# Performance work log

Measured on AMD Instinct MI355X. Metric: run time of the kernel, lower is better.

## Reference

```python
import jax, jax.numpy as jnp
import numpy as np

DIM, HEADS, K = 128, 4, 7
HD = DIM // HEADS


def _nbr_idx(n, k):
    # NATTEN boundary-clamped neighborhood (dilation=1): window start clamped to [0, n-k]
    i = np.arange(n)
    start = np.clip(i - k // 2, 0, n - k)
    idx = start[:, None] + np.arange(k)[None, :]          # (n, k) absolute neighbor index
    rel = idx - i[:, None] + (k - 1)                      # (n, k) index into 2k-1 rpb axis
    return jnp.asarray(idx), jnp.asarray(rel)


def _ln(x, w, b, eps=1e-5):
    mu = jnp.mean(x, -1, keepdims=True)
    var = jnp.var(x, -1, keepdims=True)
    return (x - mu) * jax.lax.rsqrt(var + eps) * w + b


def setup_inputs() -> dict:
    key = jax.random.key(0)
    ks = jax.random.split(key, 16)
    B, H, W, C = 1, 128, 128, DIM
    f = jax.random.normal
    inp = {
        'x': f(ks[0], (B, H, W, C), jnp.float32),
        'y': f(ks[1], (B, H, W, C), jnp.float32),
        'qv_w': f(ks[2], (2 * C, C), jnp.float32) * 0.02,
        'qv_b': jnp.zeros((2 * C,), jnp.float32),
        'k_w': f(ks[3], (C, C), jnp.float32) * 0.02,
        'k_b': jnp.zeros((C,), jnp.float32),
        'rpb': f(ks[4], (HEADS, 2 * K - 1, 2 * K - 1), jnp.float32) * 0.02,
        'proj_w': f(ks[5], (C, C), jnp.float32) * 0.02,
        'proj_b': jnp.zeros((C,), jnp.float32),
        'n1_w': jnp.ones((C,), jnp.float32),
        'n1_b': jnp.zeros((C,), jnp.float32),
        'n2_w': jnp.ones((C,), jnp.float32),
        'n2_b': jnp.zeros((C,), jnp.float32),
        'fc1_w': f(ks[6], (4 * C, C), jnp.float32) * 0.02,
        'fc1_b': jnp.zeros((4 * C,), jnp.float32),
        'fc2_w': f(ks[7], (C, 4 * C), jnp.float32) * 0.02,
        'fc2_b': jnp.zeros((C,), jnp.float32),
    }
    return inp


def _block(x, y, qv_w, qv_b, k_w, k_b, rpb, proj_w, proj_b,
           n1_w, n1_b, n2_w, n2_b, fc1_w, fc1_b, fc2_w, fc2_b):
    B, H, W, C = x.shape
    scale = HD ** -0.5
    # ---- CrossNat2D attention on norm1(x) vs y ----
    xn = _ln(x, n1_w, n1_b)
    qv = xn @ qv_w.T + qv_b                               # (B,H,W,2C)
    q = qv[..., :C].reshape(B, H, W, HEADS, HD) * scale
    v = qv[..., C:].reshape(B, H, W, HEADS, HD)
    k = (y @ k_w.T + k_b).reshape(B, H, W, HEADS, HD)

    idx_h, rel_h = _nbr_idx(H, K)
    idx_w, rel_w = _nbr_idx(W, K)
    # gather neighborhoods: (B, H, K, W, K, HEADS, HD)
    k_nbr = k[:, idx_h][:, :, :, idx_w]
    v_nbr = v[:, idx_h][:, :, :, idx_w]

    # attention logits over KxK neighborhood
    attn = jnp.einsum('bijhd,biajchd->bijhac', q, k_nbr)  # (B,H,W,heads,K,K)
    bias = rpb[:, rel_h][..., rel_w]                      # (heads,H,K,W,K)
    attn = attn + jnp.transpose(bias, (1, 3, 0, 2, 4))    # broadcast over B
    attn = jax.nn.softmax(attn.reshape(B, H, W, HEADS, K * K), axis=-1)
    attn = attn.reshape(B, H, W, HEADS, K, K)

    out = jnp.einsum('bijhac,biajchd->bijhd', attn, v_nbr).reshape(B, H, W, C)
    out = out @ proj_w.T + proj_b

    x = x + out
    # ---- MLP ----
    h = _ln(x, n2_w, n2_b) @ fc1_w.T + fc1_b
    h = jax.nn.gelu(h, approximate=False) @ fc2_w.T + fc2_b
    return x + h


def reference(x, y, qv_w, qv_b, k_w, k_b, rpb, proj_w, proj_b,
              n1_w, n1_b, n2_w, n2_b, fc1_w, fc1_b, fc2_w, fc2_b):
    return _block(x, y, qv_w, qv_b, k_w, k_b, rpb, proj_w, proj_b,
                  n1_w, n1_b, n2_w, n2_b, fc1_w, fc1_b, fc2_w, fc2_b)
```

## Files before the change

kernel.cpp:

```cpp
#include <hip/hip_runtime.h>
#include <hip/hip_bf16.h>


#define N_PIX 16384
#define C 128
#define HEADS 4
#define HD 32
#define HW 128

typedef __hip_bfloat16 bf16;
typedef __attribute__((ext_vector_type(8))) short bf16x8;
typedef __attribute__((ext_vector_type(4))) float f32x4;

__device__ __forceinline__ short f2bs(float f) {
    bf16 h = __float2bfloat16(f);
    return (short)__bfloat16_as_ushort(h);
}
__device__ __forceinline__ float bs2f(short s) {
    __hip_bfloat16_raw r; r.x = (unsigned short)s;
    return __bfloat162float(__hip_bfloat16(r));
}
__device__ __forceinline__ float gelu_f(float v) {
    const float z = 1.5957691216f * (v + 0.044715f * v * v * v);
    return v / (1.f + __expf(-z));
}
__device__ __forceinline__ unsigned int pack2(float a, float b) {
    return (unsigned int)(unsigned short)f2bs(a) |
           ((unsigned int)(unsigned short)f2bs(b) << 16);
}

__global__ __launch_bounds__(256) void k_wconv(
    const float* __restrict__ qv_w, const float* __restrict__ k_w,
    const float* __restrict__ proj_w, const float* __restrict__ fc1_w,
    const float* __restrict__ fc2_w,
    short* __restrict__ wqv, short* __restrict__ wk, short* __restrict__ wproj,
    short* __restrict__ wfc1, short* __restrict__ wfc2) {
    const int i = blockIdx.x * 256 + threadIdx.x;
    if (i < 32768) wqv[i] = f2bs(qv_w[i]);
    if (i < 16384) { wk[i] = f2bs(k_w[i]); wproj[i] = f2bs(proj_w[i]); }
    if (i < 65536) { wfc1[i] = f2bs(fc1_w[i]); wfc2[i] = f2bs(fc2_w[i]); }
}

__global__ __launch_bounds__(256, 4) void k_qkv(
    const float* __restrict__ x, const float* __restrict__ y,
    const short* __restrict__ wqv, const float* __restrict__ qv_b,
    const short* __restrict__ wk, const float* __restrict__ k_b,
    const float* __restrict__ n1_w, const float* __restrict__ n1_b,
    bf16* __restrict__ qb, bf16* __restrict__ vb, bf16* __restrict__ kb) {
    __shared__ float xr[16][132];
    __shared__ short xn[16][136];
    __shared__ short yl[16][136];
    __shared__ float muA[16], riA[16];
    const int t = threadIdx.x;
    const int pix0 = (blockIdx.x & 7) * 2048 + (blockIdx.x >> 3) * 16;
    for (int e = t; e < 512; e += 256) {
        const int r = e >> 5, c4 = (e & 31) * 4;
        const float4 xv = *(const float4*)(x + (size_t)(pix0 + r) * C + c4);
        *(float4*)&xr[r][c4] = xv;
        const float4 yv = *(const float4*)(y + (size_t)(pix0 + r) * C + c4);
        uint2 yp; yp.x = pack2(yv.x, yv.y); yp.y = pack2(yv.z, yv.w);
        *(uint2*)&yl[r][c4] = yp;
    }
    __syncthreads();
    if (t < 128) {
        const int r = t >> 3, s = t & 7;
        float sm = 0.f, sq = 0.f;
        for (int i = 0; i < 16; i++) { float v = xr[r][s * 16 + i]; sm += v; sq += v * v; }
        for (int m = 1; m < 8; m <<= 1) { sm += __shfl_xor(sm, m, 64); sq += __shfl_xor(sq, m, 64); }
        if (s == 0) {
            const float mu = sm * (1.f / 128.f);
            const float var = sq * (1.f / 128.f) - mu * mu;
            muA[r] = mu; riA[r] = rsqrtf(var + 1e-5f);
        }
    }
    __syncthreads();
    for (int e = t; e < 2048; e += 256) {
        const int r = e >> 7, c = e & 127;
        xn[r][c] = f2bs((xr[r][c] - muA[r]) * riA[r] * n1_w[c] + n1_b[c]);
    }
    __syncthreads();
    const int wave = t >> 6, lane = t & 63, quad = lane >> 4, l15 = lane & 15;
    const float scale = 0.1767766952966369f;
    {
        bf16x8 aA[4];
#pragma unroll
        for (int kt = 0; kt < 4; kt++)
            aA[kt] = *(const bf16x8*)&xn[l15][kt * 32 + quad * 8];
#pragma unroll
        for (int s = 0; s < 4; s++) {
            const int n = (wave * 4 + s) * 16 + l15;
            f32x4 acc = {0.f, 0.f, 0.f, 0.f};
#pragma unroll
            for (int kt = 0; kt < 4; kt++) {
                bf16x8 b = *(const bf16x8*)&wqv[n * C + kt * 32 + quad * 8];
                acc = __builtin_amdgcn_mfma_f32_16x16x32_bf16(aA[kt], b, acc, 0, 0, 0);
            }
            const float bias = qv_b[n];
#pragma unroll
            for (int r = 0; r < 4; r++) {
                const int m = quad * 4 + r;
                const float v = acc[r] + bias;
                if (n < C) qb[(size_t)(pix0 + m) * C + n] = __float2bfloat16(v * scale);
                else       vb[(size_t)(pix0 + m) * C + (n - C)] = __float2bfloat16(v);
            }
        }
    }
    {
        bf16x8 aY[4];
#pragma unroll
        for (int kt = 0; kt < 4; kt++)
            aY[kt] = *(const bf16x8*)&yl[l15][kt * 32 + quad * 8];
        const int n0 = (wave * 2) * 16 + l15, n1 = (wave * 2 + 1) * 16 + l15;
        f32x4 a0 = {0.f, 0.f, 0.f, 0.f}, a1 = {0.f, 0.f, 0.f, 0.f};
#pragma unroll
        for (int kt = 0; kt < 4; kt++) {
            bf16x8 b0 = *(const bf16x8*)&wk[n0 * C + kt * 32 + quad * 8];
            bf16x8 b1 = *(const bf16x8*)&wk[n1 * C + kt * 32 + quad * 8];
            a0 = __builtin_amdgcn_mfma_f32_16x16x32_bf16(aY[kt], b0, a0, 0, 0, 0);
            a1 = __builtin_amdgcn_mfma_f32_16x16x32_bf16(aY[kt], b1, a1, 0, 0, 0);
        }
        const float b0s = k_b[n0], b1s = k_b[n1];
#pragma unroll
        for (int r = 0; r < 4; r++) {
            const int m = quad * 4 + r;
            kb[(size_t)(pix0 + m) * C + n0] = __float2bfloat16(a0[r] + b0s);
            kb[(size_t)(pix0 + m) * C + n1] = __float2bfloat16(a1[r] + b1s);
        }
    }
}

__global__ __launch_bounds__(512, 2) void k_fam(
    const bf16* __restrict__ qb, const bf16* __restrict__ kb,
    const bf16* __restrict__ vb, const float* __restrict__ rpb,
    const float* __restrict__ x,
    const short* __restrict__ wproj, const float* __restrict__ proj_b,
    const float* __restrict__ n2_w, const float* __restrict__ n2_b,
    const short* __restrict__ wfc1, const float* __restrict__ fc1_b,
    const short* __restrict__ wfc2, const float* __restrict__ fc2_b,
    float* __restrict__ out) {
    __shared__ short KP[19008];
    __shared__ short Vl[19008];
    __shared__ float muA[32], riA[32];
    short* const Pm  = KP;
    short* const aoL = KP;
    short* const x1b = KP + 4352;
    short* const xnb = KP + 8704;
    short* const hb  = Vl;
    const int t = threadIdx.x;
    const int wave = t >> 6, lane = t & 63, quad = lane >> 4, l15 = lane & 15;
    const int h = wave & 3, mt = wave >> 2;
    const int s_ = blockIdx.x >> 3;
    const int i0 = ((blockIdx.x & 7) * 2 + (s_ >> 5)) * 8;
    const int j0 = (s_ & 31) * 4;
    const int rs = min(max(i0 - 3, 0), 114);
    const int cs = min(max(j0 - 3, 0), 118);
    const int mA = mt * 16 + l15;
    const int pA = (i0 + (mA >> 2)) * HW + j0 + (mA & 3);
    const bf16x8 aQ = *(const bf16x8*)(qb + (size_t)pA * C + h * HD + quad * 8);
    const int nR0 = h * 16 + l15, nR1 = (h + 4) * 16 + l15;
    float xres0[4], xres1[4];
#pragma unroll
    for (int r = 0; r < 4; r++) {
        const int m = mt * 16 + quad * 4 + r;
        const int p = (i0 + (m >> 2)) * HW + j0 + (m & 3);
        xres0[r] = x[(size_t)p * C + nR0];
        xres1[r] = x[(size_t)p * C + nR1];
    }
    for (int u = t; u < 140 * 16 * 2; u += 512) {
        const int tv = (u >= 2240) ? 1 : 0;
        const int uu = tv ? u - 2240 : u;
        const int r = uu >> 4, seg = uu & 15;
        const size_t g = (size_t)((rs + r / 10) * HW + cs + r % 10) * C + seg * 8;
        const uint4 d = *(const uint4*)((tv ? vb : kb) + g);
        *(uint4*)&(tv ? Vl : KP)[r * 132 + seg * 8] = d;
    }
    __syncthreads();
    f32x4 S[9];
#pragma unroll
    for (int nt = 0; nt < 9; nt++) {
        const bf16x8 bK = *(const bf16x8*)&KP[(nt * 16 + l15) * 132 + h * HD + quad * 8];
        f32x4 z = {0.f, 0.f, 0.f, 0.f};
        S[nt] = __builtin_amdgcn_mfma_f32_16x16x32_bf16(aQ, bK, z, 0, 0, 0);
    }
    const float* rpbh = rpb + h * 169;
    float smx[4];
#pragma unroll
    for (int r = 0; r < 4; r++) {
        const int m = mt * 16 + quad * 4 + r;
        const int i = i0 + (m >> 2), j = j0 + (m & 3);
        const int shi = min(max(i - 3, 0), 121);
        const int swj = min(max(j - 3, 0), 121);
        float best = -1e30f;
#pragma unroll
        for (int nt = 0; nt < 9; nt++) {
            const int nb = nt * 16 + l15;
            const int ai = rs + nb / 10, aj = cs + nb % 10;
            const bool valid = (nb < 140) & (ai >= shi) & (ai <= shi + 6) & (aj >= swj) & (aj <= swj + 6);
            const int ri = min(max(ai - i + 6, 0), 12);
            const int rj = min(max(aj - j + 6, 0), 12);
            const float v = valid ? (S[nt][r] + rpbh[ri * 13 + rj]) : -1e30f;
            S[nt][r] = v;
            best = fmaxf(best, v);
        }
        for (int msk = 1; msk < 16; msk <<= 1) best = fmaxf(best, __shfl_xor(best, msk, 64));
        float s = 0.f;
#pragma unroll
        for (int nt = 0; nt < 9; nt++) {
            const float e = __expf(S[nt][r] - best);
            S[nt][r] = e;
            s += e;
        }
        for (int msk = 1; msk < 16; msk <<= 1) s += __shfl_xor(s, msk, 64);
        smx[r] = 1.f / s;
    }
    __syncthreads();
#pragma unroll
    for (int r = 0; r < 4; r++) {
        short* prow = &Pm[(wave * 16 + quad * 4 + r) * 144];
#pragma unroll
        for (int nt = 0; nt < 9; nt++)
            prow[nt * 16 + l15] = f2bs(S[nt][r] * smx[r]);
    }
    f32x4 O0 = {0.f, 0.f, 0.f, 0.f}, O1 = {0.f, 0.f, 0.f, 0.f};
#pragma unroll
    for (int kt = 0; kt < 4; kt++) {
        const bf16x8 aP = *(const bf16x8*)&Pm[(wave * 16 + l15) * 144 + kt * 32 + quad * 8];
#pragma unroll
        for (int nt2 = 0; nt2 < 2; nt2++) {
            const int ch = h * HD + nt2 * 16 + l15;
            const int base = (kt * 32 + quad * 8) * 132 + ch;
            bf16x8 bV;
#pragma unroll
            for (int jj = 0; jj < 8; jj++) bV[jj] = Vl[base + jj * 132];
            if (nt2 == 0) O0 = __builtin_amdgcn_mfma_f32_16x16x32_bf16(aP, bV, O0, 0, 0, 0);
            else          O1 = __builtin_amdgcn_mfma_f32_16x16x32_bf16(aP, bV, O1, 0, 0, 0);
        }
    }
    {
        const bf16x8 aP = *(const bf16x8*)&Pm[(wave * 16 + l15) * 144 + 128 + quad * 8];
#pragma unroll
        for (int nt2 = 0; nt2 < 2; nt2++) {
            const int ch = h * HD + nt2 * 16 + l15;
            bf16x8 bV = {0, 0, 0, 0, 0, 0, 0, 0};
            if (quad == 0) {
                const int base = 128 * 132 + ch;
#pragma unroll
                for (int jj = 0; jj < 8; jj++) bV[jj] = Vl[base + jj * 132];
            } else if (quad == 1) {
                const int base = 136 * 132 + ch;
#pragma unroll
                for (int jj = 0; jj < 4; jj++) bV[jj] = Vl[base + jj * 132];
            }
            if (nt2 == 0) O0 = __builtin_amdgcn_mfma_f32_16x16x32_bf16(aP, bV, O0, 0, 0, 0);
            else          O1 = __builtin_amdgcn_mfma_f32_16x16x32_bf16(aP, bV, O1, 0, 0, 0);
        }
    }
    __syncthreads();
#pragma unroll
    for (int r = 0; r < 4; r++) {
        const int m = mt * 16 + quad * 4 + r;
        aoL[m * 136 + h * HD + l15] = f2bs(O0[r]);
        aoL[m * 136 + h * HD + 16 + l15] = f2bs(O1[r]);
    }
    __syncthreads();
    float x1f0[4], x1f1[4];
    {
        bf16x8 aO[4];
#pragma unroll
        for (int kt = 0; kt < 4; kt++)
            aO[kt] = *(const bf16x8*)&aoL[(mt * 16 + l15) * 136 + kt * 32 + quad * 8];
        f32x4 a0 = {0.f, 0.f, 0.f, 0.f}, a1 = {0.f, 0.f, 0.f, 0.f};
#pragma unroll
        for (int kt = 0; kt < 4; kt++) {
            bf16x8 b0 = *(const bf16x8*)&wproj[nR0 * C + kt * 32 + quad * 8];
            bf16x8 b1 = *(const bf16x8*)&wproj[nR1 * C + kt * 32 + quad * 8];
            a0 = __builtin_amdgcn_mfma_f32_16x16x32_bf16(aO[kt], b0, a0, 0, 0, 0);
            a1 = __builtin_amdgcn_mfma_f32_16x16x32_bf16(aO[kt], b1, a1, 0, 0, 0);
        }
        const float b0s = proj_b[nR0], b1s = proj_b[nR1];
#pragma unroll
        for (int r = 0; r < 4; r++) {
            const int m = mt * 16 + quad * 4 + r;
            const float v0 = xres0[r] + a0[r] + b0s;
            const float v1 = xres1[r] + a1[r] + b1s;
            x1f0[r] = v0; x1f1[r] = v1;
            x1b[m * 136 + nR0] = f2bs(v0);
            x1b[m * 136 + nR1] = f2bs(v1);
        }
    }
    __syncthreads();
    if (t < 256) {
        const int r = t >> 3, s = t & 7;
        float sm = 0.f, sq = 0.f;
        for (int i = 0; i < 16; i++) { float v = bs2f(x1b[r * 136 + s * 16 + i]); sm += v; sq += v * v; }
        for (int m = 1; m < 8; m <<= 1) { sm += __shfl_xor(sm, m, 64); sq += __shfl_xor(sq, m, 64); }
        if (s == 0) {
            const float mu = sm * (1.f / 128.f);
            const float var = sq * (1.f / 128.f) - mu * mu;
            muA[r] = mu; riA[r] = rsqrtf(var + 1e-5f);
        }
    }
    __syncthreads();
    for (int e = t; e < 32 * 128; e += 512) {
        const int r = e >> 7, c = e & 127;
        xnb[r * 136 + c] = f2bs((bs2f(x1b[r * 136 + c]) - muA[r]) * riA[r] * n2_w[c] + n2_b[c]);
    }
    __syncthreads();
    {
        bf16x8 aX[4];
#pragma unroll
        for (int kt = 0; kt < 4; kt++)
            aX[kt] = *(const bf16x8*)&xnb[(mt * 16 + l15) * 136 + kt * 32 + quad * 8];
#pragma unroll
        for (int a = 0; a < 4; a++) {
            const int n0 = (h + 8 * a) * 16 + l15, n1 = (h + 8 * a + 4) * 16 + l15;
            f32x4 a0 = {0.f, 0.f, 0.f, 0.f}, a1 = {0.f, 0.f, 0.f, 0.f};
#pragma unroll
            for (int kt = 0; kt < 4; kt++) {
                bf16x8 b0 = *(const bf16x8*)&wfc1[n0 * C + kt * 32 + quad * 8];
                bf16x8 b1 = *(const bf16x8*)&wfc1[n1 * C + kt * 32 + quad * 8];
                a0 = __builtin_amdgcn_mfma_f32_16x16x32_bf16(aX[kt], b0, a0, 0, 0, 0);
                a1 = __builtin_amdgcn_mfma_f32_16x16x32_bf16(aX[kt], b1, a1, 0, 0, 0);
            }
            const float b0s = fc1_b[n0], b1s = fc1_b[n1];
#pragma unroll
            for (int r = 0; r < 4; r++) {
                const int m = mt * 16 + quad * 4 + r;
                hb[m * 520 + n0] = f2bs(gelu_f(a0[r] + b0s));
                hb[m * 520 + n1] = f2bs(gelu_f(a1[r] + b1s));
            }
        }
    }
    __syncthreads();
    {
        f32x4 a0 = {0.f, 0.f, 0.f, 0.f}, a1 = {0.f, 0.f, 0.f, 0.f};
#pragma unroll
        for (int kt = 0; kt < 16; kt++) {
            const bf16x8 aP = *(const bf16x8*)&hb[(mt * 16 + l15) * 520 + kt * 32 + quad * 8];
            bf16x8 b0 = *(const bf16x8*)&wfc2[nR0 * 512 + kt * 32 + quad * 8];
            bf16x8 b1 = *(const bf16x8*)&wfc2[nR1 * 512 + kt * 32 + quad * 8];
            a0 = __builtin_amdgcn_mfma_f32_16x16x32_bf16(aP, b0, a0, 0, 0, 0);
            a1 = __builtin_amdgcn_mfma_f32_16x16x32_bf16(aP, b1, a1, 0, 0, 0);
        }
        const float b0s = fc2_b[nR0], b1s = fc2_b[nR1];
#pragma unroll
        for (int r = 0; r < 4; r++) {
            const int m = mt * 16 + quad * 4 + r;
            const int p = (i0 + (m >> 2)) * HW + j0 + (m & 3);
            out[(size_t)p * C + nR0] = a0[r] + b0s + x1f0[r];
            out[(size_t)p * C + nR1] = a1[r] + b1s + x1f1[r];
        }
    }
}

extern "C" void kernel_launch(void* const* d_in, const int* in_sizes, int n_in,
                              void* d_out, int out_size, void* d_ws, size_t ws_size,
                              hipStream_t stream) {
    const float* x      = (const float*)d_in[0];
    const float* y      = (const float*)d_in[1];
    const float* qv_w   = (const float*)d_in[2];
    const float* qv_b   = (const float*)d_in[3];
    const float* k_w    = (const float*)d_in[4];
    const float* k_b    = (const float*)d_in[5];
    const float* rpb    = (const float*)d_in[6];
    const float* proj_w = (const float*)d_in[7];
    const float* proj_b = (const float*)d_in[8];
    const float* n1_w   = (const float*)d_in[9];
    const float* n1_b   = (const float*)d_in[10];
    const float* n2_w   = (const float*)d_in[11];
    const float* n2_b   = (const float*)d_in[12];
    const float* fc1_w  = (const float*)d_in[13];
    const float* fc1_b  = (const float*)d_in[14];
    const float* fc2_w  = (const float*)d_in[15];
    const float* fc2_b  = (const float*)d_in[16];
    float* out = (float*)d_out;

    bf16* qb  = (bf16*)d_ws;
    bf16* vb  = qb + (size_t)N_PIX * C;
    bf16* kb  = vb + (size_t)N_PIX * C;
    short* wqv  = (short*)(kb + (size_t)N_PIX * C);
    short* wk   = wqv + 32768;
    short* wproj= wk + 16384;
    short* wfc1 = wproj + 16384;
    short* wfc2 = wfc1 + 65536;

    k_wconv<<<256, 256, 0, stream>>>(qv_w, k_w, proj_w, fc1_w, fc2_w,
                                     wqv, wk, wproj, wfc1, wfc2);
    k_qkv<<<1024, 256, 0, stream>>>(x, y, wqv, qv_b, wk, k_b, n1_w, n1_b,
                                    qb, vb, kb);
    k_fam<<<512, 512, 0, stream>>>(qb, kb, vb, rpb, x, wproj, proj_b, n2_w, n2_b,
                                   wfc1, fc1_b, wfc2, fc2_b, out);
}
```

Measured before the change: 160.1 us.

## Micro-optimize conversions, LayerNorm reductions, gather indexing, and raise k_fam occupancy

Swaps the bf16 conversions for a packed v_cvt_pk_bf16_f32 instruction and rewrites GELU to use exp2f with folded constants. Spreads both LayerNorm stat reductions over all threads with vectorized loads, and replaces the div/mod neighborhood load and index math with incremental counters. Prefetches proj weights before a barrier and raises k_fam launch bounds to 4 blocks per CU, which may force register spills. The fused kernel's LDS use (~76KB per block) likely caps real occupancy anyway.

```diff
diff --git a/kernel.cpp b/kernel.cpp
--- a/kernel.cpp
+++ b/kernel.cpp
@@ -13,20 +13,22 @@
 typedef __attribute__((ext_vector_type(4))) float f32x4;
 
 __device__ __forceinline__ short f2bs(float f) {
-    bf16 h = __float2bfloat16(f);
-    return (short)__bfloat16_as_ushort(h);
+    unsigned int r;
+    asm("v_cvt_pk_bf16_f32 %0, %1, %2" : "=v"(r) : "v"(f), "v"(f));
+    return (short)(r & 0xffff);
+}
+__device__ __forceinline__ unsigned int pack2(float a, float b) {
+    unsigned int r;
+    asm("v_cvt_pk_bf16_f32 %0, %1, %2" : "=v"(r) : "v"(a), "v"(b));
+    return r;
 }
 __device__ __forceinline__ float bs2f(short s) {
     __hip_bfloat16_raw r; r.x = (unsigned short)s;
     return __bfloat162float(__hip_bfloat16(r));
 }
 __device__ __forceinline__ float gelu_f(float v) {
-    const float z = 1.5957691216f * (v + 0.044715f * v * v * v);
-    return v / (1.f + __expf(-z));
-}
-__device__ __forceinline__ unsigned int pack2(float a, float b) {
-    return (unsigned int)(unsigned short)f2bs(a) |
-           ((unsigned int)(unsigned short)f2bs(b) << 16);
+    const float z2 = v * (2.302236206f + 0.102943322f * v * v);
+    return v / (1.f + exp2f(-z2));
 }
 
 __global__ __launch_bounds__(256) void k_wconv(
@@ -62,12 +64,18 @@
         *(uint2*)&yl[r][c4] = yp;
     }
     __syncthreads();
-    if (t < 128) {
-        const int r = t >> 3, s = t & 7;
-        float sm = 0.f, sq = 0.f;
-        for (int i = 0; i < 16; i++) { float v = xr[r][s * 16 + i]; sm += v; sq += v * v; }
-        for (int m = 1; m < 8; m <<= 1) { sm += __shfl_xor(sm, m, 64); sq += __shfl_xor(sq, m, 64); }
-        if (s == 0) {
+    {
+        const int r = t >> 4, c8 = (t & 15) * 8;
+        const float4 a = *(const float4*)&xr[r][c8];
+        const float4 b = *(const float4*)&xr[r][c8 + 4];
+        float sm = a.x + a.y + a.z + a.w + b.x + b.y + b.z + b.w;
+        float sq = a.x * a.x + a.y * a.y + a.z * a.z + a.w * a.w
+                 + b.x * b.x + b.y * b.y + b.z * b.z + b.w * b.w;
+#pragma unroll
+        for (int msk = 1; msk < 16; msk <<= 1) {
+            sm += __shfl_xor(sm, msk, 64); sq += __shfl_xor(sq, msk, 64);
+        }
+        if ((t & 15) == 0) {
             const float mu = sm * (1.f / 128.f);
             const float var = sq * (1.f / 128.f) - mu * mu;
             muA[r] = mu; riA[r] = rsqrtf(var + 1e-5f);
@@ -129,7 +137,7 @@
     }
 }
 
-__global__ __launch_bounds__(512, 2) void k_fam(
+__global__ __launch_bounds__(512, 4) void k_fam(
     const bf16* __restrict__ qb, const bf16* __restrict__ kb,
     const bf16* __restrict__ vb, const float* __restrict__ rpb,
     const float* __restrict__ x,
@@ -166,13 +174,25 @@
         xres0[r] = x[(size_t)p * C + nR0];
         xres1[r] = x[(size_t)p * C + nR1];
     }
-    for (int u = t; u < 140 * 16 * 2; u += 512) {
-        const int tv = (u >= 2240) ? 1 : 0;
-        const int uu = tv ? u - 2240 : u;
-        const int r = uu >> 4, seg = uu & 15;
-        const size_t g = (size_t)((rs + r / 10) * HW + cs + r % 10) * C + seg * 8;
-        const uint4 d = *(const uint4*)((tv ? vb : kb) + g);
-        *(uint4*)&(tv ? Vl : KP)[r * 132 + seg * 8] = d;
+    {
+        const int seg = t & 15, r0 = t >> 4;
+        const int q0 = (r0 * 13) >> 7;
+        const int m0 = r0 - q0 * 10;
+#pragma unroll
+        for (int half = 0; half < 2; half++) {
+            const bf16* __restrict__ src = half ? vb : kb;
+            short* const dst = half ? Vl : KP;
+            int r = r0, q = q0, rm = m0;
+#pragma unroll
+            for (int it = 0; it < 5; it++) {
+                if (r < 140) {
+                    const size_t g = (size_t)((rs + q) * HW + cs + rm) * C + seg * 8;
+                    *(uint4*)&dst[r * 132 + seg * 8] = *(const uint4*)(src + g);
+                }
+                r += 32; q += 3; rm += 2;
+                if (rm >= 10) { rm -= 10; q += 1; }
+            }
+        }
     }
     __syncthreads();
     f32x4 S[9];
@@ -183,6 +203,18 @@
         S[nt] = __builtin_amdgcn_mfma_f32_16x16x32_bf16(aQ, bK, z, 0, 0, 0);
     }
     const float* rpbh = rpb + h * 169;
+    int aiA[9], ajA[9];
+    {
+        int ai = rs + (l15 >= 10 ? 1 : 0);
+        int aj = cs + (l15 >= 10 ? l15 - 10 : l15);
+        const int cb = cs + 10;
+#pragma unroll
+        for (int nt = 0; nt < 9; nt++) {
+            aiA[nt] = ai; ajA[nt] = aj;
+            aj += 6; ai += 1;
+            if (aj >= cb) { aj -= 10; ai += 1; }
+        }
+    }
     float smx[4];
 #pragma unroll
     for (int r = 0; r < 4; r++) {
@@ -193,9 +225,9 @@
         float best = -1e30f;
 #pragma unroll
         for (int nt = 0; nt < 9; nt++) {
-            const int nb = nt * 16 + l15;
-            const int ai = rs + nb / 10, aj = cs + nb % 10;
-            const bool valid = (nb < 140) & (ai >= shi) & (ai <= shi + 6) & (aj >= swj) & (aj <= swj + 6);
+            const int ai = aiA[nt], aj = ajA[nt];
+            const bool vnb = (nt < 8) | (l15 < 12);
+            const bool valid = vnb & (ai >= shi) & (ai <= shi + 6) & (aj >= swj) & (aj <= swj + 6);
             const int ri = min(max(ai - i + 6, 0), 12);
             const int rj = min(max(aj - j + 6, 0), 12);
             const float v = valid ? (S[nt][r] + rpbh[ri * 13 + rj]) : -1e30f;
@@ -255,6 +287,12 @@
             else          O1 = __builtin_amdgcn_mfma_f32_16x16x32_bf16(aP, bV, O1, 0, 0, 0);
         }
     }
+    bf16x8 wp0[4], wp1[4];
+#pragma unroll
+    for (int kt = 0; kt < 4; kt++) {
+        wp0[kt] = *(const bf16x8*)&wproj[nR0 * C + kt * 32 + quad * 8];
+        wp1[kt] = *(const bf16x8*)&wproj[nR1 * C + kt * 32 + quad * 8];
+    }
     __syncthreads();
 #pragma unroll
     for (int r = 0; r < 4; r++) {
@@ -272,10 +310,8 @@
         f32x4 a0 = {0.f, 0.f, 0.f, 0.f}, a1 = {0.f, 0.f, 0.f, 0.f};
 #pragma unroll
         for (int kt = 0; kt < 4; kt++) {
-            bf16x8 b0 = *(const bf16x8*)&wproj[nR0 * C + kt * 32 + quad * 8];
-            bf16x8 b1 = *(const bf16x8*)&wproj[nR1 * C + kt * 32 + quad * 8];
-            a0 = __builtin_amdgcn_mfma_f32_16x16x32_bf16(aO[kt], b0, a0, 0, 0, 0);
-            a1 = __builtin_amdgcn_mfma_f32_16x16x32_bf16(aO[kt], b1, a1, 0, 0, 0);
+            a0 = __builtin_amdgcn_mfma_f32_16x16x32_bf16(aO[kt], wp0[kt], a0, 0, 0, 0);
+            a1 = __builtin_amdgcn_mfma_f32_16x16x32_bf16(aO[kt], wp1[kt], a1, 0, 0, 0);
         }
         const float b0s = proj_b[nR0], b1s = proj_b[nR1];
 #pragma unroll
@@ -289,12 +325,19 @@
         }
     }
     __syncthreads();
-    if (t < 256) {
-        const int r = t >> 3, s = t & 7;
+    {
+        const int r = t >> 4, c8 = (t & 15) * 8;
+        const short* p = &x1b[r * 136 + c8];
         float sm = 0.f, sq = 0.f;
-        for (int i = 0; i < 16; i++) { float v = bs2f(x1b[r * 136 + s * 16 + i]); sm += v; sq += v * v; }
-        for (int m = 1; m < 8; m <<= 1) { sm += __shfl_xor(sm, m, 64); sq += __shfl_xor(sq, m, 64); }
-        if (s == 0) {
+#pragma unroll
+        for (int i2 = 0; i2 < 8; i2++) {
+            const float v = bs2f(p[i2]); sm += v; sq += v * v;
+        }
+#pragma unroll
+        for (int msk = 1; msk < 16; msk <<= 1) {
+            sm += __shfl_xor(sm, msk, 64); sq += __shfl_xor(sq, msk, 64);
+        }
+        if ((t & 15) == 0) {
             const float mu = sm * (1.f / 128.f);
             const float var = sq * (1.f / 128.f) - mu * mu;
             muA[r] = mu; riA[r] = rsqrtf(var + 1e-5f);
```

Measured after the change: 161.1 us. No clear change (+0.6%).
